# Optimization experiments

Measured on AMD Instinct MI355X. Metric: run time of the kernel, lower is better.

## Reference

```python
import jax, jax.numpy as jnp
import numpy as np

B, IN, COND, HID, LAT, E = 8192, 512, 256, 1024, 128, 4
EPS = 1e-4  # RunningMeanStd epsilon

def leaky(x):
    return jax.nn.leaky_relu(x, 0.01)

def _norm(a, m, v):
    # RunningMeanStd.normalize: clip((a-mean)/sqrt(var+eps), -5, 5)
    return jnp.clip((a - m) / jnp.sqrt(v + EPS), -5.0, 5.0)

def setup_inputs() -> dict:
    key = jax.random.key(0)
    ks = iter(jax.random.split(key, 64))
    def rn(shape, scale=0.02):
        return jax.random.normal(next(ks), shape, dtype=jnp.float32) * scale
    z32 = lambda *s: jnp.zeros(s, jnp.float32)
    return {
        'x': rn((B, IN), 1.0), 'w': rn((B, COND), 1.0), 'eps': rn((B, LAT), 1.0),
        'rms_in_mean': z32(IN), 'rms_in_var': jnp.ones((IN,), jnp.float32),
        'rms_c_mean': z32(COND), 'rms_c_var': jnp.ones((COND,), jnp.float32),
        'enc_w0': rn((IN + COND, HID)), 'enc_b0': z32(HID),
        'enc_w1': rn((COND + HID, HID)), 'enc_b1': z32(HID),
        'enc_w2': rn((COND + HID, HID)), 'enc_b2': z32(HID),
        'enc_w3': rn((COND + HID, HID)), 'enc_b3': z32(HID),
        'mu_w': rn((HID, LAT)), 'mu_b': z32(LAT),
        'lv_w': rn((HID, LAT)), 'lv_b': z32(LAT),
        'g_w0': rn((LAT + COND, 64)), 'g_b0': z32(64),
        'g_w1': rn((64, 64)), 'g_b1': z32(64),
        'g_w2': rn((64, E)), 'g_b2': z32(E),
        'dec_w0': rn((E, LAT + COND, HID)), 'dec_b0': jnp.full((E, HID), 0.01, jnp.float32),
        'dec_w1': rn((E, LAT + COND + HID, HID)), 'dec_b1': jnp.full((E, HID), 0.01, jnp.float32),
        'dec_w2': rn((E, LAT + COND + HID, HID)), 'dec_b2': jnp.full((E, HID), 0.01, jnp.float32),
        'dec_w3': rn((E, LAT + COND + HID, HID)), 'dec_b3': jnp.full((E, HID), 0.01, jnp.float32),
        'dec_w4': rn((E, LAT + COND + HID, IN)), 'dec_b4': jnp.full((E, IN), 0.01, jnp.float32),
    }

def _forward(x, w, eps, rms_in_mean, rms_in_var, rms_c_mean, rms_c_var,
             enc_w0, enc_b0, enc_w1, enc_b1, enc_w2, enc_b2, enc_w3, enc_b3,
             mu_w, mu_b, lv_w, lv_b,
             g_w0, g_b0, g_w1, g_b1, g_w2, g_b2,
             dec_w0, dec_b0, dec_w1, dec_b1, dec_w2, dec_b2, dec_w3, dec_b3,
             dec_w4, dec_b4):
    xn = _norm(x, rms_in_mean, rms_in_var)
    wn = _norm(w, rms_c_mean, rms_c_var)
    wn = jnp.where(jnp.isnan(wn), 0.0, wn)
    # encoder: original encode() loop applies ONLY the Linear ops (LeakyReLUs skipped),
    # concatenating w before every Linear after the first
    h = jnp.concatenate([xn, wn], -1) @ enc_w0 + enc_b0
    for W, b in ((enc_w1, enc_b1), (enc_w2, enc_b2), (enc_w3, enc_b3)):
        h = jnp.concatenate([wn, h], -1) @ W + b
    mu = leaky(h) @ mu_w + mu_b
    log_var = jnp.clip(leaky(h) @ lv_w + lv_b, -5.0, 5.0)
    z = mu + eps * jnp.exp(0.5 * log_var)  # reparameterize
    # MixedDecoder: gate -> softmax coefficients over experts
    c = wn
    g = leaky(jnp.concatenate([z, c], -1) @ g_w0 + g_b0)
    g = leaky(g @ g_w1 + g_b1)
    coeff = jax.nn.softmax(g @ g_w2 + g_b2, axis=-1)  # [B, E]
    out = c
    layers = ((dec_w0, dec_b0, True), (dec_w1, dec_b1, True),
              (dec_w2, dec_b2, True), (dec_w3, dec_b3, True),
              (dec_w4, dec_b4, False))
    for i, (W, b, act) in enumerate(layers):
        inp = jnp.concatenate([z, out], -1) if i == 0 else jnp.concatenate([z, c, out], -1)
        # fused soft-MoE: sum_e coeff_e * (inp @ W_e) + coeff @ b_e
        he = jnp.einsum('bi,eio->beo', inp, W)          # [B, E, out_dim]
        o = jnp.einsum('beo,be->bo', he, coeff) + coeff @ b
        out = leaky(o) if act else o
    return z, out, mu, log_var

def reference(x, w, eps, rms_in_mean, rms_in_var, rms_c_mean, rms_c_var,
              enc_w0, enc_b0, enc_w1, enc_b1, enc_w2, enc_b2, enc_w3, enc_b3,
              mu_w, mu_b, lv_w, lv_b,
              g_w0, g_b0, g_w1, g_b1, g_w2, g_b2,
              dec_w0, dec_b0, dec_w1, dec_b1, dec_w2, dec_b2, dec_w3, dec_b3,
              dec_w4, dec_b4):
    return _forward(x, w, eps, rms_in_mean, rms_in_var, rms_c_mean, rms_c_var,
                    enc_w0, enc_b0, enc_w1, enc_b1, enc_w2, enc_b2, enc_w3, enc_b3,
                    mu_w, mu_b, lv_w, lv_b,
                    g_w0, g_b0, g_w1, g_b1, g_w2, g_b2,
                    dec_w0, dec_b0, dec_w1, dec_b1, dec_w2, dec_b2, dec_w3, dec_b3,
                    dec_w4, dec_b4)
```

## Files before the change

kernel.cpp:

```cpp
#include <hip/hip_runtime.h>

#define BATCH 8192

typedef __bf16 bf16x8 __attribute__((ext_vector_type(8)));
typedef float f32x4 __attribute__((ext_vector_type(4)));
typedef float f32x16 __attribute__((ext_vector_type(16)));

__device__ __forceinline__ float leakyf(float x) { return x > 0.f ? x : 0.01f * x; }

__device__ __forceinline__ short f2bf(float f) {
    union { float f; unsigned u; } v; v.f = f;
    unsigned r = v.u + 0x7fffu + ((v.u >> 16) & 1u);
    return (short)(r >> 16);
}
__device__ __forceinline__ float bf2f(short s) {
    union { unsigned u; float f; } v; v.u = ((unsigned)(unsigned short)s) << 16;
    return v.f;
}

__global__ __launch_bounds__(256) void transconv_k(const float* __restrict__ in,
                                                   short* __restrict__ out,
                                                   int R, int C, int ldo) {
    __shared__ float t[32][33];
    const int r0 = blockIdx.y * 32, c0 = blockIdx.x * 32;
    const int tx = threadIdx.x, ty = threadIdx.y;
#pragma unroll
    for (int i = 0; i < 4; ++i)
        t[ty * 4 + i][tx] = in[(size_t)(r0 + ty * 4 + i) * C + c0 + tx];
    __syncthreads();
#pragma unroll
    for (int i = 0; i < 4; ++i)
        out[(size_t)(c0 + ty * 4 + i) * ldo + r0 + tx] = f2bf(t[tx][ty * 4 + i]);
}

__global__ __launch_bounds__(256) void transconv_moe_k(const float* __restrict__ in,
                                                       short* __restrict__ out, int C) {
    __shared__ float t[32][33];
    const int r0 = blockIdx.y * 32, c0 = blockIdx.x * 32;
    const int tx = threadIdx.x, ty = threadIdx.y;
#pragma unroll
    for (int i = 0; i < 4; ++i)
        t[ty * 4 + i][tx] = in[(size_t)(r0 + ty * 4 + i) * C + c0 + tx];
    __syncthreads();
    const int e = r0 / 1408, k = r0 - e * 1408;
    const int rp0 = (k < 384) ? (e * 384 + k) : (1536 + e * 1024 + (k - 384));
#pragma unroll
    for (int i = 0; i < 4; ++i)
        out[(size_t)(c0 + ty * 4 + i) * 5632 + rp0 + tx] = f2bf(t[tx][ty * 4 + i]);
}

template <int BM, int EPI>
__global__ __launch_bounds__(512) void mm_p3(
    const short* __restrict__ A, int lda,
    const short* __restrict__ Bt, int ldb,
    const float* __restrict__ bias, const float* __restrict__ coeff,
    short* __restrict__ Cb, float* __restrict__ Cf, int ldc, int N, int K) {
    constexpr int TSZA = BM * 64;
    constexpr int TSZB = 128 * 64;
    constexpr int RA = BM / 64;
    constexpr int WMR = BM / 4;
    constexpr int AF = WMR / 32;
    __shared__ short As[3 * TSZA];
    __shared__ short Bs[2 * TSZB];
    const int tid = threadIdx.x;
    const int wave = tid >> 6, lane = tid & 63;
    const int wm = wave >> 1, wq = wave & 1;

    int bx = blockIdx.x, by = blockIdx.y;
    {
        int nwg = gridDim.x * gridDim.y;
        if ((nwg & 7) == 0) {
            int flat = by * gridDim.x + bx;
            int nf = (flat & 7) * (nwg >> 3) + (flat >> 3);
            bx = nf % gridDim.x;
            by = nf / gridDim.x;
        }
    }
    const int m0 = by * BM, n0 = bx * 128;
    const int srow = lane >> 3;
    const int scolsw = ((lane & 7) ^ srow) << 3;
    const int l31 = lane & 31;
    const int kh32 = (lane >> 5) << 3;

    auto stageA = [&](int kt, int buf) {
#pragma unroll
        for (int it = 0; it < RA; ++it) {
            int chunk = it * 8 + wave;
            int row = chunk * 8 + srow;
            const short* g = A + (size_t)(m0 + row) * lda + kt + scolsw;
            __builtin_amdgcn_global_load_lds(
                (const __attribute__((address_space(1))) void*)g,
                (__attribute__((address_space(3))) void*)(As + buf * TSZA + chunk * 512),
                16, 0, 0);
        }
    };
    auto stageB = [&](int kt, int buf) {
#pragma unroll
        for (int it = 0; it < 2; ++it) {
            int chunk = it * 8 + wave;
            int row = chunk * 8 + srow;
            const short* g = Bt + (size_t)(n0 + row) * ldb + kt + scolsw;
            __builtin_amdgcn_global_load_lds(
                (const __attribute__((address_space(1))) void*)g,
                (__attribute__((address_space(3))) void*)(Bs + buf * TSZB + chunk * 512),
                16, 0, 0);
        }
    };
    auto waitRA = [&]() {
        if constexpr (BM == 256) {
            asm volatile("s_waitcnt vmcnt(4)" ::: "memory");
        } else {
            asm volatile("s_waitcnt vmcnt(2)" ::: "memory");
        }
    };

    f32x16 acc[AF][2];
#pragma unroll
    for (int i = 0; i < AF; ++i)
#pragma unroll
        for (int j = 0; j < 2; ++j)
#pragma unroll
            for (int r = 0; r < 16; ++r) acc[i][j][r] = 0.f;

    const int nk = K >> 6;

    stageA(0, 0);
    stageB(0, 0);
    stageA(64, 1);
    __builtin_amdgcn_sched_barrier(0);
    waitRA();
    __builtin_amdgcn_s_barrier();
    __builtin_amdgcn_sched_barrier(0);

    int ia = 0;
    int is = 2;
#pragma unroll 1
    for (int t = 0; t < nk; ++t) {
        const short* Ah = As + ia * TSZA;
        const short* Bh = Bs + (t & 1) * TSZB;

        {
            bf16x8 a[AF][2], b[2][2];
#pragma unroll
            for (int s = 0; s < 2; ++s) {
#pragma unroll
                for (int i = 0; i < AF; ++i) {
                    int R = wm * WMR + i * 32 + l31;
                    a[i][s] = *(const bf16x8*)&Ah[R * 64 + ((s * 16 + kh32) ^ ((R & 7) << 3))];
                }
#pragma unroll
                for (int j = 0; j < 2; ++j) {
                    int R = wq * 64 + j * 32 + l31;
                    b[j][s] = *(const bf16x8*)&Bh[R * 64 + ((s * 16 + kh32) ^ ((R & 7) << 3))];
                }
            }
            if (t + 1 < nk) stageB((t + 1) << 6, (t + 1) & 1);
            __builtin_amdgcn_sched_barrier(0);
            __builtin_amdgcn_s_barrier();
            __builtin_amdgcn_s_setprio(1);
#pragma unroll
            for (int s = 0; s < 2; ++s)
#pragma unroll
                for (int i = 0; i < AF; ++i)
#pragma unroll
                    for (int j = 0; j < 2; ++j)
                        acc[i][j] = __builtin_amdgcn_mfma_f32_32x32x16_bf16(
                            a[i][s], b[j][s], acc[i][j], 0, 0, 0);
            __builtin_amdgcn_s_setprio(0);
            __builtin_amdgcn_sched_barrier(0);
            __builtin_amdgcn_s_barrier();
        }

        {
            bf16x8 a[AF][2], b[2][2];
#pragma unroll
            for (int s = 0; s < 2; ++s) {
#pragma unroll
                for (int i = 0; i < AF; ++i) {
                    int R = wm * WMR + i * 32 + l31;
                    a[i][s] = *(const bf16x8*)&Ah[R * 64 + (((s + 2) * 16 + kh32) ^ ((R & 7) << 3))];
                }
#pragma unroll
                for (int j = 0; j < 2; ++j) {
                    int R = wq * 64 + j * 32 + l31;
                    b[j][s] = *(const bf16x8*)&Bh[R * 64 + (((s + 2) * 16 + kh32) ^ ((R & 7) << 3))];
                }
            }
            if (t + 2 < nk) stageA((t + 2) << 6, is);
            __builtin_amdgcn_sched_barrier(0);
            __builtin_amdgcn_s_barrier();
            __builtin_amdgcn_s_setprio(1);
#pragma unroll
            for (int s = 0; s < 2; ++s)
#pragma unroll
                for (int i = 0; i < AF; ++i)
#pragma unroll
                    for (int j = 0; j < 2; ++j)
                        acc[i][j] = __builtin_amdgcn_mfma_f32_32x32x16_bf16(
                            a[i][s], b[j][s], acc[i][j], 0, 0, 0);
            __builtin_amdgcn_s_setprio(0);
            __builtin_amdgcn_sched_barrier(0);
            if (t + 1 < nk) {
                if (t + 2 < nk) {
                    waitRA();
                } else {
                    asm volatile("s_waitcnt vmcnt(0)" ::: "memory");
                }
            }
            __builtin_amdgcn_s_barrier();
        }
        ia = (ia == 2) ? 0 : ia + 1;
        is = (is == 2) ? 0 : is + 1;
    }

#pragma unroll
    for (int i = 0; i < AF; ++i) {
#pragma unroll
        for (int g = 0; g < 4; ++g) {
#pragma unroll
            for (int r = 0; r < 4; ++r) {
                int reg = g * 4 + r;
                int row = m0 + wm * WMR + i * 32 + g * 8 + ((lane >> 5) << 2) + r;
#pragma unroll
                for (int j = 0; j < 2; ++j) {
                    int col = n0 + wq * 64 + j * 32 + l31;
                    float v = acc[i][j][reg];
                    if constexpr (EPI == 0) {
                        v += bias[col];
                        Cb[(size_t)row * ldc + col] = f2bf(v);
                    } else if constexpr (EPI == 1) {
                        v = leakyf(v + bias[col]);
                        Cb[(size_t)row * ldc + col] = f2bf(v);
                    } else if constexpr (EPI == 5) {
                        const float4 c4 = *reinterpret_cast<const float4*>(coeff + (size_t)row * 4);
                        v += c4.x * bias[col] + c4.y * bias[N + col] +
                             c4.z * bias[2 * N + col] + c4.w * bias[3 * N + col];
                        float a = leakyf(v);
                        Cb[(size_t)row * ldc + 0 * 1024 + col] = f2bf(c4.x * a);
                        Cb[(size_t)row * ldc + 1 * 1024 + col] = f2bf(c4.y * a);
                        Cb[(size_t)row * ldc + 2 * 1024 + col] = f2bf(c4.z * a);
                        Cb[(size_t)row * ldc + 3 * 1024 + col] = f2bf(c4.w * a);
                    } else {
                        const float4 c4 = *reinterpret_cast<const float4*>(coeff + (size_t)row * 4);
                        v += c4.x * bias[col] + c4.y * bias[N + col] +
                             c4.z * bias[2 * N + col] + c4.w * bias[3 * N + col];
                        Cf[(size_t)row * ldc + col] = v;
                    }
                }
            }
        }
    }
}

template <int BM, int BN, int EPI>
__global__ __launch_bounds__(256) void mm_k(
    const short* __restrict__ A, int lda,
    const short* __restrict__ Bt, int ldb,
    const float* __restrict__ bias, const float* __restrict__ bias2,
    const float* __restrict__ coeff,
    short* __restrict__ Cb, float* __restrict__ Cf, float* __restrict__ Cf2,
    int ldc, int N, int K) {
    constexpr bool MOE = (EPI == 3 || EPI == 4);
    constexpr int WM = BM / 2, WN = BN / 2;
    constexpr int FM = WM / 16, FN = WN / 16;
    constexpr int ASZ = BM * 64, BSZ = BN * 64;
    __shared__ short As[2 * ASZ];
    __shared__ short Bs[2 * BSZ];
    const int tid = threadIdx.x;
    const int wave = tid >> 6, lane = tid & 63;
    const int wm = wave >> 1, wq = wave & 1;

    int bx = blockIdx.x, by = blockIdx.y;
    {
        int nwg = gridDim.x * gridDim.y;
        if ((nwg & 7) == 0) {
            int flat = by * gridDim.x + bx;
            int nf = (flat & 7) * (nwg >> 3) + (flat >> 3);
            bx = nf % gridDim.x;
            by = nf / gridDim.x;
        }
    }
    const int m0 = by * BM, n0 = bx * BN;
    const int srow = lane >> 3;
    const int scolsw = ((lane & 7) ^ srow) << 3;
    const int l15 = lane & 15;
    const int khalf = (lane >> 4) << 3;

    auto stage = [&](const short* Bsrc, int kt, int half) {
#pragma unroll
        for (int it = 0; it < BM / 32; ++it) {
            int chunk = it * 4 + wave;
            int row = chunk * 8 + srow;
            const short* g = A + (size_t)(m0 + row) * lda + kt + scolsw;
            __builtin_amdgcn_global_load_lds(
                (const __attribute__((address_space(1))) void*)g,
                (__attribute__((address_space(3))) void*)(As + half * ASZ + chunk * 512),
                16, 0, 0);
        }
#pragma unroll
        for (int it = 0; it < BN / 32; ++it) {
            int chunk = it * 4 + wave;
            int row = chunk * 8 + srow;
            const short* g = Bsrc + (size_t)(n0 + row) * ldb + kt + scolsw;
            __builtin_amdgcn_global_load_lds(
                (const __attribute__((address_space(1))) void*)g,
                (__attribute__((address_space(3))) void*)(Bs + half * BSZ + chunk * 512),
                16, 0, 0);
        }
    };

    f32x4 acc[FM][FN];
    f32x4 accf[MOE ? FM : 1][MOE ? FN : 1];
    const f32x4 z4 = {0.f, 0.f, 0.f, 0.f};
    if constexpr (MOE) {
#pragma unroll
        for (int i = 0; i < FM; ++i)
#pragma unroll
            for (int j = 0; j < FN; ++j) accf[i][j] = z4;
    }

    constexpr int NE = MOE ? 4 : 1;
    const int nk = K >> 6;
#pragma unroll 1
    for (int e = 0; e < NE; ++e) {
        const short* Be = Bt + (size_t)e * K;
#pragma unroll
        for (int i = 0; i < FM; ++i)
#pragma unroll
            for (int j = 0; j < FN; ++j) acc[i][j] = z4;

        stage(Be, 0, 0);
        __syncthreads();

#pragma unroll 1
        for (int t = 0; t < nk; ++t) {
            const int cur = t & 1;
            if (t + 1 < nk) stage(Be, (t + 1) << 6, cur ^ 1);
            const short* Ah = As + cur * ASZ;
            const short* Bh = Bs + cur * BSZ;
#pragma unroll
            for (int kk = 0; kk < 2; ++kk) {
                bf16x8 a[FM], b[FN];
#pragma unroll
                for (int i = 0; i < FM; ++i) {
                    int R = wm * WM + i * 16 + l15;
                    int off = (kk * 32 + khalf) ^ ((R & 7) << 3);
                    a[i] = *(const bf16x8*)&Ah[R * 64 + off];
                }
#pragma unroll
                for (int j = 0; j < FN; ++j) {
                    int R = wq * WN + j * 16 + l15;
                    int off = (kk * 32 + khalf) ^ ((R & 7) << 3);
                    b[j] = *(const bf16x8*)&Bh[R * 64 + off];
                }
#pragma unroll
                for (int i = 0; i < FM; ++i)
#pragma unroll
                    for (int j = 0; j < FN; ++j)
                        acc[i][j] = __builtin_amdgcn_mfma_f32_16x16x32_bf16(
                            a[i], b[j], acc[i][j], 0, 0, 0);
            }
            __syncthreads();
        }
        if constexpr (MOE) {
#pragma unroll
            for (int i = 0; i < FM; ++i) {
                int rbase = m0 + wm * WM + i * 16 + ((lane >> 4) << 2);
#pragma unroll
                for (int r = 0; r < 4; ++r) {
                    float ce = coeff[(size_t)(rbase + r) * 4 + e];
#pragma unroll
                    for (int j = 0; j < FN; ++j) accf[i][j][r] += ce * acc[i][j][r];
                }
            }
        }
    }

#pragma unroll
    for (int i = 0; i < FM; ++i) {
#pragma unroll
        for (int r = 0; r < 4; ++r) {
            int row = m0 + wm * WM + i * 16 + ((lane >> 4) << 2) + r;
#pragma unroll
            for (int j = 0; j < FN; ++j) {
                int col = n0 + wq * WN + j * 16 + l15;
                float v = MOE ? accf[i][j][r] : acc[i][j][r];
                if constexpr (EPI == 0) {
                    v += bias[col];
                    Cb[(size_t)row * ldc + col] = f2bf(v);
                } else if constexpr (EPI == 1) {
                    v = leakyf(v + bias[col]);
                    Cb[(size_t)row * ldc + col] = f2bf(v);
                } else if constexpr (EPI == 2) {
                    if (col < 128) {
                        Cf[(size_t)row * 128 + col] = v + bias[col];
                    } else {
                        float u = v + bias2[col - 128];
                        u = fminf(fmaxf(u, -5.f), 5.f);
                        Cf2[(size_t)row * 128 + (col - 128)] = u;
                    }
                } else if constexpr (EPI == 3) {
                    const float* c4 = coeff + (size_t)row * 4;
                    v += c4[0] * bias[col] + c4[1] * bias[N + col] +
                         c4[2] * bias[2 * N + col] + c4[3] * bias[3 * N + col];
                    Cb[(size_t)row * ldc + col] = f2bf(leakyf(v));
                } else {
                    const float* c4 = coeff + (size_t)row * 4;
                    v += c4[0] * bias[col] + c4[1] * bias[N + col] +
                         c4[2] * bias[2 * N + col] + c4[3] * bias[3 * N + col];
                    Cf[(size_t)row * ldc + col] = v;
                }
            }
        }
    }
}

__global__ __launch_bounds__(256) void norm_k(
    const float* __restrict__ x, const float* __restrict__ w,
    const float* __restrict__ im, const float* __restrict__ iv,
    const float* __restrict__ cm, const float* __restrict__ cv,
    short* __restrict__ enc0, short* __restrict__ encA,
    short* __restrict__ encB, short* __restrict__ dec0) {
    int idx = blockIdx.x * 256 + threadIdx.x;
    const int TX = BATCH * 512;
    if (idx < TX) {
        int b = idx >> 9, j = idx & 511;
        float v = (x[idx] - im[j]) * rsqrtf(iv[j] + 1e-4f);
        v = fminf(fmaxf(v, -5.f), 5.f);
        enc0[(size_t)b * 768 + j] = f2bf(v);
    } else {
        int k = idx - TX;
        if (k < BATCH * 256) {
            int b = k >> 8, j = k & 255;
            float v = (w[k] - cm[j]) * rsqrtf(cv[j] + 1e-4f);
            if (v != v) v = 0.f;
            v = fminf(fmaxf(v, -5.f), 5.f);
            short s = f2bf(v);
            enc0[(size_t)b * 768 + 512 + j] = s;
            encA[(size_t)b * 1280 + j] = s;
            encB[(size_t)b * 1280 + j] = s;
            dec0[(size_t)b * 384 + 128 + j] = s;
        }
    }
}

__global__ __launch_bounds__(256) void reparam_k(
    const float* __restrict__ mu, const float* __restrict__ lv,
    const float* __restrict__ eps, float* __restrict__ z, short* __restrict__ dec0) {
    int idx = blockIdx.x * 256 + threadIdx.x;
    if (idx >= BATCH * 128) return;
    float zv = mu[idx] + eps[idx] * expf(0.5f * lv[idx]);
    z[idx] = zv;
    int b = idx >> 7, j = idx & 127;
    dec0[(size_t)b * 384 + j] = f2bf(zv);
}

__global__ __launch_bounds__(256) void fill_zc_k(const short* __restrict__ dec0,
                                                 const float* __restrict__ cf,
                                                 short* __restrict__ dA,
                                                 short* __restrict__ dB) {
    int idx = blockIdx.x * 256 + threadIdx.x;
    if (idx >= BATCH * 1536) return;
    int b = idx / 1536, c = idx - b * 1536;
    int e = c / 384, k = c - e * 384;
    short s = f2bf(cf[(size_t)b * 4 + e] * bf2f(dec0[(size_t)b * 384 + k]));
    dA[(size_t)b * 5632 + c] = s;
    dB[(size_t)b * 5632 + c] = s;
}

__global__ __launch_bounds__(256) void fill_dec_k(const short* __restrict__ dec0,
                                                  short* __restrict__ decA,
                                                  short* __restrict__ decB) {
    int idx = blockIdx.x * 256 + threadIdx.x;
    if (idx >= BATCH * 384) return;
    int b = idx / 384, c = idx - b * 384;
    short s = dec0[idx];
    decA[(size_t)b * 1408 + c] = s;
    decB[(size_t)b * 1408 + c] = s;
}

__global__ __launch_bounds__(256) void gate_sm_k(const short* __restrict__ g1,
                                                 const float* __restrict__ w2,
                                                 const float* __restrict__ b2,
                                                 float* __restrict__ coeff) {
    int r = blockIdx.x * 256 + threadIdx.x;
    if (r >= BATCH) return;
    float l0 = b2[0], l1 = b2[1], l2 = b2[2], l3 = b2[3];
    const short* row = g1 + (size_t)r * 64;
#pragma unroll
    for (int k = 0; k < 64; ++k) {
        float gv = bf2f(row[k]);
        l0 += gv * w2[k * 4 + 0];
        l1 += gv * w2[k * 4 + 1];
        l2 += gv * w2[k * 4 + 2];
        l3 += gv * w2[k * 4 + 3];
    }
    float mx = fmaxf(fmaxf(l0, l1), fmaxf(l2, l3));
    float e0 = expf(l0 - mx), e1 = expf(l1 - mx), e2 = expf(l2 - mx), e3 = expf(l3 - mx);
    float s = 1.f / (e0 + e1 + e2 + e3);
    float4 outv = make_float4(e0 * s, e1 * s, e2 * s, e3 * s);
    *reinterpret_cast<float4*>(coeff + (size_t)r * 4) = outv;
}

extern "C" void kernel_launch(void* const* d_in, const int* in_sizes, int n_in,
                              void* d_out, int out_size, void* d_ws, size_t ws_size,
                              hipStream_t stream) {
    const float* x    = (const float*)d_in[0];
    const float* w    = (const float*)d_in[1];
    const float* epsv = (const float*)d_in[2];
    const float* rim  = (const float*)d_in[3];
    const float* riv  = (const float*)d_in[4];
    const float* rcm  = (const float*)d_in[5];
    const float* rcv  = (const float*)d_in[6];
    const float* ew0 = (const float*)d_in[7];  const float* eb0 = (const float*)d_in[8];
    const float* ew1 = (const float*)d_in[9];  const float* eb1 = (const float*)d_in[10];
    const float* ew2 = (const float*)d_in[11]; const float* eb2 = (const float*)d_in[12];
    const float* ew3 = (const float*)d_in[13]; const float* eb3 = (const float*)d_in[14];
    const float* muw = (const float*)d_in[15]; const float* mub = (const float*)d_in[16];
    const float* lvw = (const float*)d_in[17]; const float* lvb = (const float*)d_in[18];
    const float* gw0 = (const float*)d_in[19]; const float* gb0 = (const float*)d_in[20];
    const float* gw1 = (const float*)d_in[21]; const float* gb1 = (const float*)d_in[22];
    const float* gw2 = (const float*)d_in[23]; const float* gb2 = (const float*)d_in[24];
    const float* dw0 = (const float*)d_in[25]; const float* db0 = (const float*)d_in[26];
    const float* dw1 = (const float*)d_in[27]; const float* db1 = (const float*)d_in[28];
    const float* dw2 = (const float*)d_in[29]; const float* db2 = (const float*)d_in[30];
    const float* dw3 = (const float*)d_in[31]; const float* db3 = (const float*)d_in[32];
    const float* dw4 = (const float*)d_in[33]; const float* db4 = (const float*)d_in[34];

    float* out    = (float*)d_out;
    float* z_out  = out;
    float* y_out  = out + (size_t)BATCH * 128;
    float* mu_out = out + (size_t)BATCH * 640;
    float* lv_out = out + (size_t)BATCH * 768;

    char* cur = (char*)d_ws;
    auto alloc = [&](size_t bytes) -> char* {
        char* p = cur;
        cur += (bytes + 255) & ~(size_t)255;
        return p;
    };
    auto align256 = [](size_t b) { return (b + 255) & ~(size_t)255; };

    short* ew0t = (short*)alloc((size_t)768 * 1024 * 2);
    short* ew1t = (short*)alloc((size_t)1280 * 1024 * 2);
    short* ew2t = (short*)alloc((size_t)1280 * 1024 * 2);
    short* ew3t = (short*)alloc((size_t)1280 * 1024 * 2);
    short* hdWt = (short*)alloc((size_t)256 * 1024 * 2);
    short* gw0t = (short*)alloc((size_t)64 * 384 * 2);
    short* gw1t = (short*)alloc((size_t)64 * 64 * 2);
    short* dw0t = (short*)alloc((size_t)1024 * 1536 * 2);
    short* dw1t = (short*)alloc((size_t)1024 * 5632 * 2);
    short* dw2t = (short*)alloc((size_t)1024 * 5632 * 2);
    short* dw3t = (short*)alloc((size_t)1024 * 5632 * 2);
    short* dw4t = (short*)alloc((size_t)512 * 5632 * 2);
    short* dec0 = (short*)alloc((size_t)BATCH * 384 * 2);
    short* g0   = (short*)alloc((size_t)BATCH * 64 * 2);
    short* g1   = (short*)alloc((size_t)BATCH * 64 * 2);
    float* cf   = (float*)alloc((size_t)BATCH * 4 * 4);

    char* region = cur;
    const size_t bigA = align256((size_t)BATCH * 5632 * 2);
    const size_t fastNeed = (size_t)(region - (char*)d_ws) + 2 * bigA;
    const bool fast = (ws_size >= fastNeed);

    short* enc0 = (short*)region;
    short* encA = (short*)(region + align256((size_t)BATCH * 768 * 2));
    short* encB = (short*)((char*)encA + align256((size_t)BATCH * 1280 * 2));
    short* hl   = encB;
    short* dAp = (short*)region;
    short* dBp = (short*)(region + bigA);
    short* decA = (short*)region;
    short* decB = (short*)(region + align256((size_t)BATCH * 1408 * 2));

    dim3 blk(256);
    dim3 blk5(512);
    dim3 tblk(32, 8);

    transconv_k<<<dim3(1024 / 32, 768 / 32), tblk, 0, stream>>>(ew0, ew0t, 768, 1024, 768);
    transconv_k<<<dim3(1024 / 32, 1280 / 32), tblk, 0, stream>>>(ew1, ew1t, 1280, 1024, 1280);
    transconv_k<<<dim3(1024 / 32, 1280 / 32), tblk, 0, stream>>>(ew2, ew2t, 1280, 1024, 1280);
    transconv_k<<<dim3(1024 / 32, 1280 / 32), tblk, 0, stream>>>(ew3, ew3t, 1280, 1024, 1280);
    transconv_k<<<dim3(128 / 32, 1024 / 32), tblk, 0, stream>>>(muw, hdWt, 1024, 128, 1024);
    transconv_k<<<dim3(128 / 32, 1024 / 32), tblk, 0, stream>>>(lvw, hdWt + (size_t)128 * 1024, 1024, 128, 1024);
    transconv_k<<<dim3(64 / 32, 384 / 32), tblk, 0, stream>>>(gw0, gw0t, 384, 64, 384);
    transconv_k<<<dim3(64 / 32, 64 / 32), tblk, 0, stream>>>(gw1, gw1t, 64, 64, 64);
    transconv_k<<<dim3(1024 / 32, 1536 / 32), tblk, 0, stream>>>(dw0, dw0t, 1536, 1024, 1536);
    if (fast) {
        transconv_moe_k<<<dim3(1024 / 32, 5632 / 32), tblk, 0, stream>>>(dw1, dw1t, 1024);
        transconv_moe_k<<<dim3(1024 / 32, 5632 / 32), tblk, 0, stream>>>(dw2, dw2t, 1024);
        transconv_moe_k<<<dim3(1024 / 32, 5632 / 32), tblk, 0, stream>>>(dw3, dw3t, 1024);
        transconv_moe_k<<<dim3(512 / 32, 5632 / 32), tblk, 0, stream>>>(dw4, dw4t, 512);
    } else {
        transconv_k<<<dim3(1024 / 32, 5632 / 32), tblk, 0, stream>>>(dw1, dw1t, 5632, 1024, 5632);
        transconv_k<<<dim3(1024 / 32, 5632 / 32), tblk, 0, stream>>>(dw2, dw2t, 5632, 1024, 5632);
        transconv_k<<<dim3(1024 / 32, 5632 / 32), tblk, 0, stream>>>(dw3, dw3t, 5632, 1024, 5632);
        transconv_k<<<dim3(512 / 32, 5632 / 32), tblk, 0, stream>>>(dw4, dw4t, 5632, 512, 5632);
    }

    norm_k<<<dim3(BATCH * 768 / 256), blk, 0, stream>>>(x, w, rim, riv, rcm, rcv,
                                                        enc0, encA, encB, dec0);

    dim3 gBig(1024 / 128, BATCH / 256);
    mm_p3<256, 0><<<gBig, blk5, 0, stream>>>(enc0, 768, ew0t, 768, eb0, nullptr,
                                             encA + 256, nullptr, 1280, 1024, 768);
    mm_p3<256, 0><<<gBig, blk5, 0, stream>>>(encA, 1280, ew1t, 1280, eb1, nullptr,
                                             encB + 256, nullptr, 1280, 1024, 1280);
    mm_p3<256, 0><<<gBig, blk5, 0, stream>>>(encB, 1280, ew2t, 1280, eb2, nullptr,
                                             encA + 256, nullptr, 1280, 1024, 1280);
    mm_p3<256, 1><<<gBig, blk5, 0, stream>>>(encA, 1280, ew3t, 1280, eb3, nullptr,
                                             hl, nullptr, 1024, 1024, 1280);

    mm_k<64, 128, 2><<<dim3(2, BATCH / 64), blk, 0, stream>>>(hl, 1024, hdWt, 1024, mub, lvb,
                                                              nullptr, nullptr, mu_out, lv_out,
                                                              0, 256, 1024);

    reparam_k<<<dim3(BATCH * 128 / 256), blk, 0, stream>>>(mu_out, lv_out, epsv, z_out, dec0);

    mm_k<64, 64, 1><<<dim3(1, BATCH / 64), blk, 0, stream>>>(dec0, 384, gw0t, 384, gb0, nullptr,
                                                             nullptr, g0, nullptr, nullptr,
                                                             64, 64, 384);
    mm_k<64, 64, 1><<<dim3(1, BATCH / 64), blk, 0, stream>>>(g0, 64, gw1t, 64, gb1, nullptr,
                                                             nullptr, g1, nullptr, nullptr,
                                                             64, 64, 64);
    gate_sm_k<<<dim3(BATCH / 256), blk, 0, stream>>>(g1, gw2, gb2, cf);

    if (fast) {
        fill_zc_k<<<dim3(BATCH * 1536 / 256), blk, 0, stream>>>(dec0, cf, dAp, dBp);
        mm_p3<256, 5><<<gBig, blk5, 0, stream>>>(dAp, 5632, dw0t, 1536, db0, cf,
                                                 dAp + 1536, nullptr, 5632, 1024, 1536);
        mm_p3<256, 5><<<gBig, blk5, 0, stream>>>(dAp, 5632, dw1t, 5632, db1, cf,
                                                 dBp + 1536, nullptr, 5632, 1024, 5632);
        mm_p3<256, 5><<<gBig, blk5, 0, stream>>>(dBp, 5632, dw2t, 5632, db2, cf,
                                                 dAp + 1536, nullptr, 5632, 1024, 5632);
        mm_p3<256, 5><<<gBig, blk5, 0, stream>>>(dAp, 5632, dw3t, 5632, db3, cf,
                                                 dBp + 1536, nullptr, 5632, 1024, 5632);
        mm_p3<128, 6><<<dim3(512 / 128, BATCH / 128), blk5, 0, stream>>>(
            dBp, 5632, dw4t, 5632, db4, cf, nullptr, y_out, 512, 512, 5632);
    } else {
        fill_dec_k<<<dim3(BATCH * 384 / 256), blk, 0, stream>>>(dec0, decA, decB);
        dim3 gDec(1024 / 128, BATCH / 128);
        mm_k<128, 128, 3><<<gDec, blk, 0, stream>>>(dec0, 384, dw0t, 1536, db0, nullptr, cf,
                                                    decA + 384, nullptr, nullptr, 1408, 1024, 384);
        mm_k<128, 128, 3><<<gDec, blk, 0, stream>>>(decA, 1408, dw1t, 5632, db1, nullptr, cf,
                                                    decB + 384, nullptr, nullptr, 1408, 1024, 1408);
        mm_k<128, 128, 3><<<gDec, blk, 0, stream>>>(decB, 1408, dw2t, 5632, db2, nullptr, cf,
                                                    decA + 384, nullptr, nullptr, 1408, 1024, 1408);
        mm_k<128, 128, 3><<<gDec, blk, 0, stream>>>(decA, 1408, dw3t, 5632, db3, nullptr, cf,
                                                    decB + 384, nullptr, nullptr, 1408, 1024, 1408);
        mm_k<128, 128, 4><<<dim3(512 / 128, BATCH / 128), blk, 0, stream>>>(
            decB, 1408, dw4t, 5632, db4, nullptr, cf, nullptr, y_out, nullptr, 512, 512, 1408);
    }
}
```

Measured before the change: 739.9 us.

## Switch mm_p3 to 16x16x32 MFMA with register double-buffered LDS fragment loads

New measurement: 718.0 us. 3.0% less time.

```diff
diff --git a/kernel.cpp b/kernel.cpp
--- a/kernel.cpp
+++ b/kernel.cpp
@@ -4,7 +4,6 @@
 
 typedef __bf16 bf16x8 __attribute__((ext_vector_type(8)));
 typedef float f32x4 __attribute__((ext_vector_type(4)));
-typedef float f32x16 __attribute__((ext_vector_type(16)));
 
 __device__ __forceinline__ float leakyf(float x) { return x > 0.f ? x : 0.01f * x; }
 
@@ -59,7 +58,7 @@
     constexpr int TSZB = 128 * 64;
     constexpr int RA = BM / 64;
     constexpr int WMR = BM / 4;
-    constexpr int AF = WMR / 32;
+    constexpr int FM = WMR / 16;
     __shared__ short As[3 * TSZA];
     __shared__ short Bs[2 * TSZB];
     const int tid = threadIdx.x;
@@ -79,8 +78,8 @@
     const int m0 = by * BM, n0 = bx * 128;
     const int srow = lane >> 3;
     const int scolsw = ((lane & 7) ^ srow) << 3;
-    const int l31 = lane & 31;
-    const int kh32 = (lane >> 5) << 3;
+    const int l15 = lane & 15;
+    const int khalf = (lane >> 4) << 3;
 
     auto stageA = [&](int kt, int buf) {
 #pragma unroll
@@ -106,21 +105,38 @@
                 16, 0, 0);
         }
     };
-    auto waitRA = [&]() {
-        if constexpr (BM == 256) {
-            asm volatile("s_waitcnt vmcnt(4)" ::: "memory");
-        } else {
-            asm volatile("s_waitcnt vmcnt(2)" ::: "memory");
+
+    f32x4 acc[FM][4];
+    const f32x4 z4 = {0.f, 0.f, 0.f, 0.f};
+#pragma unroll
+    for (int i = 0; i < FM; ++i)
+#pragma unroll
+        for (int j = 0; j < 4; ++j) acc[i][j] = z4;
+
+    auto loadA = [&](const short* Ah, int kk, bf16x8 (&a)[FM]) {
+#pragma unroll
+        for (int i = 0; i < FM; ++i) {
+            int R = wm * WMR + i * 16 + l15;
+            a[i] = *(const bf16x8*)&Ah[R * 64 + ((kk * 32 + khalf) ^ ((R & 7) << 3))];
         }
     };
-
-    f32x16 acc[AF][2];
-#pragma unroll
-    for (int i = 0; i < AF; ++i)
-#pragma unroll
-        for (int j = 0; j < 2; ++j)
-#pragma unroll
-            for (int r = 0; r < 16; ++r) acc[i][j][r] = 0.f;
+    auto loadB = [&](const short* Bh, int kk, bf16x8 (&b)[4]) {
+#pragma unroll
+        for (int j = 0; j < 4; ++j) {
+            int R = wq * 64 + j * 16 + l15;
+            b[j] = *(const bf16x8*)&Bh[R * 64 + ((kk * 32 + khalf) ^ ((R & 7) << 3))];
+        }
+    };
+    auto domfma = [&](bf16x8 (&a)[FM], bf16x8 (&b)[4]) {
+        __builtin_amdgcn_s_setprio(1);
+#pragma unroll
+        for (int i = 0; i < FM; ++i)
+#pragma unroll
+            for (int j = 0; j < 4; ++j)
+                acc[i][j] = __builtin_amdgcn_mfma_f32_16x16x32_bf16(
+                    a[i], b[j], acc[i][j], 0, 0, 0);
+        __builtin_amdgcn_s_setprio(0);
+    };
 
     const int nk = K >> 6;
 
@@ -128,9 +144,17 @@
     stageB(0, 0);
     stageA(64, 1);
     __builtin_amdgcn_sched_barrier(0);
-    waitRA();
+    if constexpr (BM == 256) {
+        asm volatile("s_waitcnt vmcnt(4)" ::: "memory");
+    } else {
+        asm volatile("s_waitcnt vmcnt(2)" ::: "memory");
+    }
     __builtin_amdgcn_s_barrier();
     __builtin_amdgcn_sched_barrier(0);
+
+    bf16x8 a0[FM], b0[4], a1[FM], b1[4];
+    loadA(As, 0, a0);
+    loadB(Bs, 0, b0);
 
     int ia = 0;
     int is = 2;
@@ -138,114 +162,66 @@
     for (int t = 0; t < nk; ++t) {
         const short* Ah = As + ia * TSZA;
         const short* Bh = Bs + (t & 1) * TSZB;
-
-        {
-            bf16x8 a[AF][2], b[2][2];
-#pragma unroll
-            for (int s = 0; s < 2; ++s) {
-#pragma unroll
-                for (int i = 0; i < AF; ++i) {
-                    int R = wm * WMR + i * 32 + l31;
-                    a[i][s] = *(const bf16x8*)&Ah[R * 64 + ((s * 16 + kh32) ^ ((R & 7) << 3))];
-                }
-#pragma unroll
-                for (int j = 0; j < 2; ++j) {
-                    int R = wq * 64 + j * 32 + l31;
-                    b[j][s] = *(const bf16x8*)&Bh[R * 64 + ((s * 16 + kh32) ^ ((R & 7) << 3))];
-                }
-            }
-            if (t + 1 < nk) stageB((t + 1) << 6, (t + 1) & 1);
-            __builtin_amdgcn_sched_barrier(0);
-            __builtin_amdgcn_s_barrier();
-            __builtin_amdgcn_s_setprio(1);
-#pragma unroll
-            for (int s = 0; s < 2; ++s)
-#pragma unroll
-                for (int i = 0; i < AF; ++i)
-#pragma unroll
-                    for (int j = 0; j < 2; ++j)
-                        acc[i][j] = __builtin_amdgcn_mfma_f32_32x32x16_bf16(
-                            a[i][s], b[j][s], acc[i][j], 0, 0, 0);
-            __builtin_amdgcn_s_setprio(0);
-            __builtin_amdgcn_sched_barrier(0);
-            __builtin_amdgcn_s_barrier();
-        }
-
-        {
-            bf16x8 a[AF][2], b[2][2];
-#pragma unroll
-            for (int s = 0; s < 2; ++s) {
-#pragma unroll
-                for (int i = 0; i < AF; ++i) {
-                    int R = wm * WMR + i * 32 + l31;
-                    a[i][s] = *(const bf16x8*)&Ah[R * 64 + (((s + 2) * 16 + kh32) ^ ((R & 7) << 3))];
-                }
-#pragma unroll
-                for (int j = 0; j < 2; ++j) {
-                    int R = wq * 64 + j * 32 + l31;
-                    b[j][s] = *(const bf16x8*)&Bh[R * 64 + (((s + 2) * 16 + kh32) ^ ((R & 7) << 3))];
-                }
-            }
-            if (t + 2 < nk) stageA((t + 2) << 6, is);
-            __builtin_amdgcn_sched_barrier(0);
-            __builtin_amdgcn_s_barrier();
-            __builtin_amdgcn_s_setprio(1);
-#pragma unroll
-            for (int s = 0; s < 2; ++s)
-#pragma unroll
-                for (int i = 0; i < AF; ++i)
-#pragma unroll
-                    for (int j = 0; j < 2; ++j)
-                        acc[i][j] = __builtin_amdgcn_mfma_f32_32x32x16_bf16(
-                            a[i][s], b[j][s], acc[i][j], 0, 0, 0);
-            __builtin_amdgcn_s_setprio(0);
-            __builtin_amdgcn_sched_barrier(0);
-            if (t + 1 < nk) {
-                if (t + 2 < nk) {
-                    waitRA();
+        const int ian = (ia == 2) ? 0 : ia + 1;
+        const short* Ah1 = As + ian * TSZA;
+        const short* Bh1 = Bs + ((t + 1) & 1) * TSZB;
+
+        loadA(Ah, 1, a1);
+        loadB(Bh, 1, b1);
+        if (t + 1 < nk) stageB((t + 1) << 6, (t + 1) & 1);
+        __builtin_amdgcn_sched_barrier(0);
+        __builtin_amdgcn_s_barrier();
+        __builtin_amdgcn_sched_barrier(0);
+        domfma(a0, b0);
+        __builtin_amdgcn_sched_barrier(0);
+        asm volatile("s_waitcnt vmcnt(0)" ::: "memory");
+        __builtin_amdgcn_s_barrier();
+        __builtin_amdgcn_sched_barrier(0);
+
+        if (t + 1 < nk) {
+            loadA(Ah1, 0, a0);
+            loadB(Bh1, 0, b0);
+        }
+        if (t + 2 < nk) stageA((t + 2) << 6, is);
+        __builtin_amdgcn_sched_barrier(0);
+        __builtin_amdgcn_s_barrier();
+        __builtin_amdgcn_sched_barrier(0);
+        domfma(a1, b1);
+        __builtin_amdgcn_sched_barrier(0);
+
+        ia = ian;
+        is = (is == 2) ? 0 : is + 1;
+    }
+
+#pragma unroll
+    for (int i = 0; i < FM; ++i) {
+#pragma unroll
+        for (int r = 0; r < 4; ++r) {
+            int row = m0 + wm * WMR + i * 16 + ((lane >> 4) << 2) + r;
+#pragma unroll
+            for (int j = 0; j < 4; ++j) {
+                int col = n0 + wq * 64 + j * 16 + l15;
+                float v = acc[i][j][r];
+                if constexpr (EPI == 0) {
+                    v += bias[col];
+                    Cb[(size_t)row * ldc + col] = f2bf(v);
+                } else if constexpr (EPI == 1) {
+                    v = leakyf(v + bias[col]);
+                    Cb[(size_t)row * ldc + col] = f2bf(v);
+                } else if constexpr (EPI == 5) {
+                    const float4 c4 = *reinterpret_cast<const float4*>(coeff + (size_t)row * 4);
+                    v += c4.x * bias[col] + c4.y * bias[N + col] +
+                         c4.z * bias[2 * N + col] + c4.w * bias[3 * N + col];
+                    float a = leakyf(v);
+                    Cb[(size_t)row * ldc + 0 * 1024 + col] = f2bf(c4.x * a);
+                    Cb[(size_t)row * ldc + 1 * 1024 + col] = f2bf(c4.y * a);
+                    Cb[(size_t)row * ldc + 2 * 1024 + col] = f2bf(c4.z * a);
+                    Cb[(size_t)row * ldc + 3 * 1024 + col] = f2bf(c4.w * a);
                 } else {
-                    asm volatile("s_waitcnt vmcnt(0)" ::: "memory");
-                }
-            }
-            __builtin_amdgcn_s_barrier();
-        }
-        ia = (ia == 2) ? 0 : ia + 1;
-        is = (is == 2) ? 0 : is + 1;
-    }
-
-#pragma unroll
-    for (int i = 0; i < AF; ++i) {
-#pragma unroll
-        for (int g = 0; g < 4; ++g) {
-#pragma unroll
-            for (int r = 0; r < 4; ++r) {
-                int reg = g * 4 + r;
-                int row = m0 + wm * WMR + i * 32 + g * 8 + ((lane >> 5) << 2) + r;
-#pragma unroll
-                for (int j = 0; j < 2; ++j) {
-                    int col = n0 + wq * 64 + j * 32 + l31;
-                    float v = acc[i][j][reg];
-                    if constexpr (EPI == 0) {
-                        v += bias[col];
-                        Cb[(size_t)row * ldc + col] = f2bf(v);
-                    } else if constexpr (EPI == 1) {
-                        v = leakyf(v + bias[col]);
-                        Cb[(size_t)row * ldc + col] = f2bf(v);
-                    } else if constexpr (EPI == 5) {
-                        const float4 c4 = *reinterpret_cast<const float4*>(coeff + (size_t)row * 4);
-                        v += c4.x * bias[col] + c4.y * bias[N + col] +
-                             c4.z * bias[2 * N + col] + c4.w * bias[3 * N + col];
-                        float a = leakyf(v);
-                        Cb[(size_t)row * ldc + 0 * 1024 + col] = f2bf(c4.x * a);
-                        Cb[(size_t)row * ldc + 1 * 1024 + col] = f2bf(c4.y * a);
-                        Cb[(size_t)row * ldc + 2 * 1024 + col] = f2bf(c4.z * a);
-                        Cb[(size_t)row * ldc + 3 * 1024 + col] = f2bf(c4.w * a);
-                    } else {
-                        const float4 c4 = *reinterpret_cast<const float4*>(coeff + (size_t)row * 4);
-                        v += c4.x * bias[col] + c4.y * bias[N + col] +
-                             c4.z * bias[2 * N + col] + c4.w * bias[3 * N + col];
-                        Cf[(size_t)row * ldc + col] = v;
-                    }
+                    const float4 c4 = *reinterpret_cast<const float4*>(coeff + (size_t)row * 4);
+                    v += c4.x * bias[col] + c4.y * bias[N + col] +
+                         c4.z * bias[2 * N + col] + c4.w * bias[3 * N + col];
+                    Cf[(size_t)row * ldc + col] = v;
                 }
             }
         }
```
